# Performance work log

Hardware: AMD Instinct MI355X
Metric: run time of the kernel (lower is better)

## Reference

```python
import jax, jax.numpy as jnp
import numpy as np

N, DEG, C_IN, C_OUT = 100000, 16, 128, 128
LN_EPS = 1e-5


def setup_inputs() -> dict:
    key = jax.random.key(0)
    k1, k2, k3, k4 = jax.random.split(key, 4)
    x = jax.random.normal(k1, (N, C_IN), dtype=jnp.float32)
    # padding index == N points at the appended zero row
    edge_index = jax.random.randint(k2, (N, DEG), 0, N + 1)
    W = jax.random.normal(k3, (C_IN, C_OUT), dtype=jnp.float32) * 0.05
    b = jax.random.normal(k4, (C_OUT,), dtype=jnp.float32) * 0.05
    eps = jnp.zeros((1,), dtype=jnp.float32)
    gamma = jnp.ones((C_OUT,), dtype=jnp.float32)
    beta = jnp.zeros((C_OUT,), dtype=jnp.float32)
    return {"x": x, "edge_index": edge_index, "W": W, "b": b,
            "eps": eps, "gamma": gamma, "beta": beta}


def reference(x, edge_index, W, b, eps, gamma, beta):
    # pad with a zero row so padding index N gathers zeros
    padded = jnp.concatenate([x, jnp.zeros((1, x.shape[1]), x.dtype)], axis=0)  # [N+1, C]
    neigh = padded[edge_index]                 # [N, DEG, C] irregular gather
    agg = neigh.sum(axis=1)                    # [N, C] neighbor sum
    h = (1.0 + eps) * x + agg                  # GIN combine
    h = h @ W + b                              # Linear
    # LayerNorm over last dim (affine, biased variance, eps=1e-5)
    mu = h.mean(axis=-1, keepdims=True)
    var = h.var(axis=-1, keepdims=True)
    out = (h - mu) * jax.lax.rsqrt(var + LN_EPS) * gamma + beta
    return out
```

## Files before the change

### kernel.cpp

```cpp
#include <hip/hip_runtime.h>
#include <stdint.h>

#define NN   100000
#define DEG  16
#define CH   128
#define TILE 64

typedef __attribute__((ext_vector_type(8))) short bf16x8;
typedef __attribute__((ext_vector_type(4))) float f32x4;

__device__ __forceinline__ uint32_t pack2_bf16(float a, float b) {
    uint32_t ua = __builtin_bit_cast(uint32_t, a);
    uint32_t ub = __builtin_bit_cast(uint32_t, b);
    ua = (ua + 0x7FFFu + ((ua >> 16) & 1u)) >> 16;
    ub = (ub + 0x7FFFu + ((ub >> 16) & 1u)) >> 16;
    return ua | (ub << 16);
}
__device__ __forceinline__ float bf_lo(uint32_t w) { return __builtin_bit_cast(float, w << 16); }
__device__ __forceinline__ float bf_hi(uint32_t w) { return __builtin_bit_cast(float, w & 0xFFFF0000u); }

__global__ __launch_bounds__(256)
void convert_x_kernel(const float* __restrict__ x, uint32_t* __restrict__ xbf) {
    const int total = NN * CH / 8;
    for (int i = blockIdx.x * blockDim.x + threadIdx.x; i < total;
         i += gridDim.x * blockDim.x) {
        float4 a = ((const float4*)x)[2 * i];
        float4 b = ((const float4*)x)[2 * i + 1];
        uint4 o;
        o.x = pack2_bf16(a.x, a.y); o.y = pack2_bf16(a.z, a.w);
        o.z = pack2_bf16(b.x, b.y); o.w = pack2_bf16(b.z, b.w);
        ((uint4*)xbf)[i] = o;
    }
    if (blockIdx.x == 0 && threadIdx.x < CH / 8)
        ((uint4*)xbf)[NN * (CH / 8) + threadIdx.x] = make_uint4(0, 0, 0, 0);
}


template <int BF>
__global__ __launch_bounds__(256, 3)
void gin_fused_kernel(const float* __restrict__ x,
                      const uint32_t* __restrict__ xbf,
                      const int*   __restrict__ edge,
                      const float* __restrict__ W,
                      const float* __restrict__ bias,
                      const float* __restrict__ epsp,
                      const float* __restrict__ gamma,
                      const float* __restrict__ beta,
                      float*       __restrict__ out)
{
    __shared__ uint32_t Wl[128 * 64];
    __shared__ uint32_t Hl[TILE * 64];

    const int t    = threadIdx.x;
    const int lane = t & 63;
    const int wv   = t >> 6;
    const int cl   = lane & 15;
    const int g4   = lane >> 4;

    #pragma unroll
    for (int j = 0; j < 32; ++j) {
        int e  = t + 256 * j;
        int n  = e & 127;
        int k2 = e >> 7;
        float a = W[(2 * k2)     * CH + n];
        float c = W[(2 * k2 + 1) * CH + n];
        Wl[n * 64 + (k2 ^ ((n & 7) << 2))] = pack2_bf16(a, c);
    }

    const float eps1 = 1.0f + epsp[0];
    float g_r[8], be_r[8], bi_r[8];
    #pragma unroll
    for (int ct = 0; ct < 8; ++ct) {
        g_r[ct]  = gamma[ct * 16 + cl];
        be_r[ct] = beta [ct * 16 + cl];
        bi_r[ct] = bias [ct * 16 + cl];
    }

    const int tile_base = blockIdx.x * TILE;
    const uint4* xb4 = (const uint4*)xbf;

    #pragma unroll
    for (int it = 0; it < 4; ++it) {
        const int row  = 16 * wv + 4 * it + g4;
        const int node = tile_base + row;
        const bool nvalid = node < NN;
        int j_all = edge[(size_t)(nvalid ? node : 0) * DEG + cl];

        float acc[8] = {0, 0, 0, 0, 0, 0, 0, 0};
        #pragma unroll
        for (int d = 0; d < DEG; ++d) {
            int j = __shfl(j_all, g4 * 16 + d, 64);
            if (BF) {
                uint4 v = xb4[(size_t)j * (CH / 8) + cl];
                acc[0] += bf_lo(v.x); acc[1] += bf_hi(v.x);
                acc[2] += bf_lo(v.y); acc[3] += bf_hi(v.y);
                acc[4] += bf_lo(v.z); acc[5] += bf_hi(v.z);
                acc[6] += bf_lo(v.w); acc[7] += bf_hi(v.w);
            } else {
                bool ok = j < NN;
                size_t jc = ok ? (size_t)j : 0;
                float4 a = ((const float4*)x)[jc * (CH / 4) + cl * 2];
                float4 b = ((const float4*)x)[jc * (CH / 4) + cl * 2 + 1];
                float m = ok ? 1.0f : 0.0f;
                acc[0] += m * a.x; acc[1] += m * a.y;
                acc[2] += m * a.z; acc[3] += m * a.w;
                acc[4] += m * b.x; acc[5] += m * b.y;
                acc[6] += m * b.z; acc[7] += m * b.w;
            }
        }
        if (BF) {
            size_t nz = nvalid ? (size_t)node : (size_t)NN;
            uint4 v = xb4[nz * (CH / 8) + cl];
            acc[0] += eps1 * bf_lo(v.x); acc[1] += eps1 * bf_hi(v.x);
            acc[2] += eps1 * bf_lo(v.y); acc[3] += eps1 * bf_hi(v.y);
            acc[4] += eps1 * bf_lo(v.z); acc[5] += eps1 * bf_hi(v.z);
            acc[6] += eps1 * bf_lo(v.w); acc[7] += eps1 * bf_hi(v.w);
        } else if (nvalid) {
            float4 a = ((const float4*)x)[(size_t)node * (CH / 4) + cl * 2];
            float4 b = ((const float4*)x)[(size_t)node * (CH / 4) + cl * 2 + 1];
            acc[0] += eps1 * a.x; acc[1] += eps1 * a.y;
            acc[2] += eps1 * a.z; acc[3] += eps1 * a.w;
            acc[4] += eps1 * b.x; acc[5] += eps1 * b.y;
            acc[6] += eps1 * b.z; acc[7] += eps1 * b.w;
        }
        uint4 hv;
        hv.x = pack2_bf16(acc[0], acc[1]); hv.y = pack2_bf16(acc[2], acc[3]);
        hv.z = pack2_bf16(acc[4], acc[5]); hv.w = pack2_bf16(acc[6], acc[7]);
        int hidx = row * 64 + ((cl * 4) ^ ((row & 7) << 2));
        ((uint4*)Hl)[hidx >> 2] = hv;
    }
    __syncthreads();

    const int arow = 16 * wv + cl;
    bf16x8 afr[4];
    #pragma unroll
    for (int ks = 0; ks < 4; ++ks) {
        int k2b = ks * 16 + g4 * 4;
        afr[ks] = *reinterpret_cast<const bf16x8*>(&Hl[arow * 64 + (k2b ^ ((arow & 7) << 2))]);
    }
    f32x4 acc[8];
    #pragma unroll
    for (int ct = 0; ct < 8; ++ct) acc[ct] = (f32x4){0.f, 0.f, 0.f, 0.f};
    #pragma unroll
    for (int ct = 0; ct < 8; ++ct) {
        int brow = ct * 16 + cl;
        #pragma unroll
        for (int ks = 0; ks < 4; ++ks) {
            int k2b = ks * 16 + g4 * 4;
            bf16x8 bfr = *reinterpret_cast<const bf16x8*>(&Wl[brow * 64 + (k2b ^ ((brow & 7) << 2))]);
            acc[ct] = __builtin_amdgcn_mfma_f32_16x16x32_bf16(afr[ks], bfr, acc[ct], 0, 0, 0);
        }
    }

    float s1[4] = {0, 0, 0, 0}, s2[4] = {0, 0, 0, 0};
    #pragma unroll
    for (int ct = 0; ct < 8; ++ct) {
        #pragma unroll
        for (int r = 0; r < 4; ++r) {
            float v = acc[ct][r] + bi_r[ct];
            acc[ct][r] = v;
            s1[r] += v;
            s2[r] += v * v;
        }
    }
    #pragma unroll
    for (int m = 1; m < 16; m <<= 1) {
        #pragma unroll
        for (int r = 0; r < 4; ++r) {
            s1[r] += __shfl_xor(s1[r], m, 64);
            s2[r] += __shfl_xor(s2[r], m, 64);
        }
    }
    #pragma unroll
    for (int r = 0; r < 4; ++r) {
        int node = tile_base + 16 * wv + g4 * 4 + r;
        if (node < NN) {
            float mu  = s1[r] * (1.0f / CH);
            float var = s2[r] * (1.0f / CH) - mu * mu;
            float rs  = rsqrtf(var + 1e-5f);
            float* op = out + (size_t)node * CH + cl;
            #pragma unroll
            for (int ct = 0; ct < 8; ++ct) {
                op[ct * 16] = (acc[ct][r] - mu) * rs * g_r[ct] + be_r[ct];
            }
        }
    }
}

extern "C" void kernel_launch(void* const* d_in, const int* in_sizes, int n_in,
                              void* d_out, int out_size, void* d_ws, size_t ws_size,
                              hipStream_t stream) {
    const float* x     = (const float*)d_in[0];
    const int*   edge  = (const int*)  d_in[1];
    const float* W     = (const float*)d_in[2];
    const float* b     = (const float*)d_in[3];
    const float* eps   = (const float*)d_in[4];
    const float* gamma = (const float*)d_in[5];
    const float* beta  = (const float*)d_in[6];
    float*       out   = (float*)d_out;

    const int grid = (NN + TILE - 1) / TILE;
    const size_t need = (size_t)(NN + 1) * CH * 2;

    if (ws_size >= need) {
        uint32_t* xbf = (uint32_t*)d_ws;
        convert_x_kernel<<<2048, 256, 0, stream>>>(x, xbf);
        gin_fused_kernel<1><<<grid, 256, 0, stream>>>(x, xbf, edge, W, b, eps, gamma, beta, out);
    } else {
        gin_fused_kernel<0><<<grid, 256, 0, stream>>>(x, nullptr, edge, W, b, eps, gamma, beta, out);
    }
}
```

Measured before the change: 82.93 us.

## Pre-convert W to bf16 once and read MFMA B-fragments from global memory

The bf16 path no longer stages W into shared memory in every block. Block 1 of the convert kernel packs W into a bf16 buffer in the workspace, and the fused kernel loads its MFMA B fragments straight from that buffer, which should stay cache-resident. This removes 32KB of LDS and the per-block conversion, so launch_bounds is raised to 7 blocks per CU for higher occupancy, and all edge-index loads are hoisted ahead of the gather loop. The cost is global/L2 traffic for W fragments in every block, and whether the occupancy hint can be met under register pressure.

```diff
diff --git a/kernel.cpp b/kernel.cpp
--- a/kernel.cpp
+++ b/kernel.cpp
@@ -20,7 +20,8 @@
 __device__ __forceinline__ float bf_hi(uint32_t w) { return __builtin_bit_cast(float, w & 0xFFFF0000u); }
 
 __global__ __launch_bounds__(256)
-void convert_x_kernel(const float* __restrict__ x, uint32_t* __restrict__ xbf) {
+void convert_kernel(const float* __restrict__ x, const float* __restrict__ W,
+                    uint32_t* __restrict__ xbf, uint32_t* __restrict__ wbf) {
     const int total = NN * CH / 8;
     for (int i = blockIdx.x * blockDim.x + threadIdx.x; i < total;
          i += gridDim.x * blockDim.x) {
@@ -33,22 +34,29 @@
     }
     if (blockIdx.x == 0 && threadIdx.x < CH / 8)
         ((uint4*)xbf)[NN * (CH / 8) + threadIdx.x] = make_uint4(0, 0, 0, 0);
-}
-
-
-template <int BF>
-__global__ __launch_bounds__(256, 3)
-void gin_fused_kernel(const float* __restrict__ x,
-                      const uint32_t* __restrict__ xbf,
-                      const int*   __restrict__ edge,
-                      const float* __restrict__ W,
-                      const float* __restrict__ bias,
-                      const float* __restrict__ epsp,
-                      const float* __restrict__ gamma,
-                      const float* __restrict__ beta,
-                      float*       __restrict__ out)
+    if (blockIdx.x == 1) {
+        #pragma unroll
+        for (int j = 0; j < 32; ++j) {
+            int e  = threadIdx.x + 256 * j;
+            int n  = e & 127;
+            int k2 = e >> 7;
+            wbf[n * 64 + k2] = pack2_bf16(W[(2 * k2) * CH + n],
+                                          W[(2 * k2 + 1) * CH + n]);
+        }
+    }
+}
+
+
+__global__ __launch_bounds__(256, 7)
+void gin_fused_bf(const uint32_t* __restrict__ xbf,
+                  const uint32_t* __restrict__ wbf,
+                  const int*   __restrict__ edge,
+                  const float* __restrict__ bias,
+                  const float* __restrict__ epsp,
+                  const float* __restrict__ gamma,
+                  const float* __restrict__ beta,
+                  float*       __restrict__ out)
 {
-    __shared__ uint32_t Wl[128 * 64];
     __shared__ uint32_t Hl[TILE * 64];
 
     const int t    = threadIdx.x;
@@ -57,16 +65,6 @@
     const int cl   = lane & 15;
     const int g4   = lane >> 4;
 
-    #pragma unroll
-    for (int j = 0; j < 32; ++j) {
-        int e  = t + 256 * j;
-        int n  = e & 127;
-        int k2 = e >> 7;
-        float a = W[(2 * k2)     * CH + n];
-        float c = W[(2 * k2 + 1) * CH + n];
-        Wl[n * 64 + (k2 ^ ((n & 7) << 2))] = pack2_bf16(a, c);
-    }
-
     const float eps1 = 1.0f + epsp[0];
     float g_r[8], be_r[8], bi_r[8];
     #pragma unroll
@@ -79,50 +77,34 @@
     const int tile_base = blockIdx.x * TILE;
     const uint4* xb4 = (const uint4*)xbf;
 
+    int jv[4];
+    #pragma unroll
+    for (int it = 0; it < 4; ++it) {
+        int node = tile_base + 16 * wv + 4 * it + g4;
+        jv[it] = edge[(size_t)(node < NN ? node : 0) * DEG + cl];
+    }
+
     #pragma unroll
     for (int it = 0; it < 4; ++it) {
         const int row  = 16 * wv + 4 * it + g4;
         const int node = tile_base + row;
-        const bool nvalid = node < NN;
-        int j_all = edge[(size_t)(nvalid ? node : 0) * DEG + cl];
-
         float acc[8] = {0, 0, 0, 0, 0, 0, 0, 0};
         #pragma unroll
         for (int d = 0; d < DEG; ++d) {
-            int j = __shfl(j_all, g4 * 16 + d, 64);
-            if (BF) {
-                uint4 v = xb4[(size_t)j * (CH / 8) + cl];
-                acc[0] += bf_lo(v.x); acc[1] += bf_hi(v.x);
-                acc[2] += bf_lo(v.y); acc[3] += bf_hi(v.y);
-                acc[4] += bf_lo(v.z); acc[5] += bf_hi(v.z);
-                acc[6] += bf_lo(v.w); acc[7] += bf_hi(v.w);
-            } else {
-                bool ok = j < NN;
-                size_t jc = ok ? (size_t)j : 0;
-                float4 a = ((const float4*)x)[jc * (CH / 4) + cl * 2];
-                float4 b = ((const float4*)x)[jc * (CH / 4) + cl * 2 + 1];
-                float m = ok ? 1.0f : 0.0f;
-                acc[0] += m * a.x; acc[1] += m * a.y;
-                acc[2] += m * a.z; acc[3] += m * a.w;
-                acc[4] += m * b.x; acc[5] += m * b.y;
-                acc[6] += m * b.z; acc[7] += m * b.w;
-            }
-        }
-        if (BF) {
-            size_t nz = nvalid ? (size_t)node : (size_t)NN;
-            uint4 v = xb4[nz * (CH / 8) + cl];
-            acc[0] += eps1 * bf_lo(v.x); acc[1] += eps1 * bf_hi(v.x);
-            acc[2] += eps1 * bf_lo(v.y); acc[3] += eps1 * bf_hi(v.y);
-            acc[4] += eps1 * bf_lo(v.z); acc[5] += eps1 * bf_hi(v.z);
-            acc[6] += eps1 * bf_lo(v.w); acc[7] += eps1 * bf_hi(v.w);
-        } else if (nvalid) {
-            float4 a = ((const float4*)x)[(size_t)node * (CH / 4) + cl * 2];
-            float4 b = ((const float4*)x)[(size_t)node * (CH / 4) + cl * 2 + 1];
-            acc[0] += eps1 * a.x; acc[1] += eps1 * a.y;
-            acc[2] += eps1 * a.z; acc[3] += eps1 * a.w;
-            acc[4] += eps1 * b.x; acc[5] += eps1 * b.y;
-            acc[6] += eps1 * b.z; acc[7] += eps1 * b.w;
-        }
+            int j = __shfl(jv[it], g4 * 16 + d, 64);
+            uint4 v = xb4[(size_t)j * (CH / 8) + cl];
+            acc[0] += bf_lo(v.x); acc[1] += bf_hi(v.x);
+            acc[2] += bf_lo(v.y); acc[3] += bf_hi(v.y);
+            acc[4] += bf_lo(v.z); acc[5] += bf_hi(v.z);
+            acc[6] += bf_lo(v.w); acc[7] += bf_hi(v.w);
+        }
+        size_t nz = (node < NN) ? (size_t)node : (size_t)NN;
+        uint4 v = xb4[nz * (CH / 8) + cl];
+        acc[0] += eps1 * bf_lo(v.x); acc[1] += eps1 * bf_hi(v.x);
+        acc[2] += eps1 * bf_lo(v.y); acc[3] += eps1 * bf_hi(v.y);
+        acc[4] += eps1 * bf_lo(v.z); acc[5] += eps1 * bf_hi(v.z);
+        acc[6] += eps1 * bf_lo(v.w); acc[7] += eps1 * bf_hi(v.w);
+
         uint4 hv;
         hv.x = pack2_bf16(acc[0], acc[1]); hv.y = pack2_bf16(acc[2], acc[3]);
         hv.z = pack2_bf16(acc[4], acc[5]); hv.w = pack2_bf16(acc[6], acc[7]);
@@ -147,7 +129,7 @@
         #pragma unroll
         for (int ks = 0; ks < 4; ++ks) {
             int k2b = ks * 16 + g4 * 4;
-            bf16x8 bfr = *reinterpret_cast<const bf16x8*>(&Wl[brow * 64 + (k2b ^ ((brow & 7) << 2))]);
+            bf16x8 bfr = *reinterpret_cast<const bf16x8*>(&wbf[brow * 64 + k2b]);
             acc[ct] = __builtin_amdgcn_mfma_f32_16x16x32_bf16(afr[ks], bfr, acc[ct], 0, 0, 0);
         }
     }
@@ -187,6 +169,132 @@
     }
 }
 
+__global__ __launch_bounds__(256, 3)
+void gin_fused_f32(const float* __restrict__ x,
+                   const int*   __restrict__ edge,
+                   const float* __restrict__ W,
+                   const float* __restrict__ bias,
+                   const float* __restrict__ epsp,
+                   const float* __restrict__ gamma,
+                   const float* __restrict__ beta,
+                   float*       __restrict__ out)
+{
+    __shared__ uint32_t Wl[128 * 64];
+    __shared__ uint32_t Hl[TILE * 64];
+
+    const int t    = threadIdx.x;
+    const int lane = t & 63;
+    const int wv   = t >> 6;
+    const int cl   = lane & 15;
+    const int g4   = lane >> 4;
+
+    #pragma unroll
+    for (int j = 0; j < 32; ++j) {
+        int e  = t + 256 * j;
+        int n  = e & 127;
+        int k2 = e >> 7;
+        Wl[n * 64 + (k2 ^ ((n & 7) << 2))] =
+            pack2_bf16(W[(2 * k2) * CH + n], W[(2 * k2 + 1) * CH + n]);
+    }
+    const float eps1 = 1.0f + epsp[0];
+    float g_r[8], be_r[8], bi_r[8];
+    #pragma unroll
+    for (int ct = 0; ct < 8; ++ct) {
+        g_r[ct]  = gamma[ct * 16 + cl];
+        be_r[ct] = beta [ct * 16 + cl];
+        bi_r[ct] = bias [ct * 16 + cl];
+    }
+    const int tile_base = blockIdx.x * TILE;
+    #pragma unroll
+    for (int it = 0; it < 4; ++it) {
+        const int row  = 16 * wv + 4 * it + g4;
+        const int node = tile_base + row;
+        const bool nvalid = node < NN;
+        int j_all = edge[(size_t)(nvalid ? node : 0) * DEG + cl];
+        float acc[8] = {0, 0, 0, 0, 0, 0, 0, 0};
+        #pragma unroll
+        for (int d = 0; d < DEG; ++d) {
+            int j = __shfl(j_all, g4 * 16 + d, 64);
+            bool ok = j < NN;
+            size_t jc = ok ? (size_t)j : 0;
+            float4 a = ((const float4*)x)[jc * (CH / 4) + cl * 2];
+            float4 b = ((const float4*)x)[jc * (CH / 4) + cl * 2 + 1];
+            float m = ok ? 1.0f : 0.0f;
+            acc[0] += m * a.x; acc[1] += m * a.y;
+            acc[2] += m * a.z; acc[3] += m * a.w;
+            acc[4] += m * b.x; acc[5] += m * b.y;
+            acc[6] += m * b.z; acc[7] += m * b.w;
+        }
+        if (nvalid) {
+            float4 a = ((const float4*)x)[(size_t)node * (CH / 4) + cl * 2];
+            float4 b = ((const float4*)x)[(size_t)node * (CH / 4) + cl * 2 + 1];
+            acc[0] += eps1 * a.x; acc[1] += eps1 * a.y;
+            acc[2] += eps1 * a.z; acc[3] += eps1 * a.w;
+            acc[4] += eps1 * b.x; acc[5] += eps1 * b.y;
+            acc[6] += eps1 * b.z; acc[7] += eps1 * b.w;
+        }
+        uint4 hv;
+        hv.x = pack2_bf16(acc[0], acc[1]); hv.y = pack2_bf16(acc[2], acc[3]);
+        hv.z = pack2_bf16(acc[4], acc[5]); hv.w = pack2_bf16(acc[6], acc[7]);
+        int hidx = row * 64 + ((cl * 4) ^ ((row & 7) << 2));
+        ((uint4*)Hl)[hidx >> 2] = hv;
+    }
+    __syncthreads();
+    const int arow = 16 * wv + cl;
+    bf16x8 afr[4];
+    #pragma unroll
+    for (int ks = 0; ks < 4; ++ks) {
+        int k2b = ks * 16 + g4 * 4;
+        afr[ks] = *reinterpret_cast<const bf16x8*>(&Hl[arow * 64 + (k2b ^ ((arow & 7) << 2))]);
+    }
+    f32x4 acc[8];
+    #pragma unroll
+    for (int ct = 0; ct < 8; ++ct) acc[ct] = (f32x4){0.f, 0.f, 0.f, 0.f};
+    #pragma unroll
+    for (int ct = 0; ct < 8; ++ct) {
+        int brow = ct * 16 + cl;
+        #pragma unroll
+        for (int ks = 0; ks < 4; ++ks) {
+            int k2b = ks * 16 + g4 * 4;
+            bf16x8 bfr = *reinterpret_cast<const bf16x8*>(&Wl[brow * 64 + (k2b ^ ((brow & 7) << 2))]);
+            acc[ct] = __builtin_amdgcn_mfma_f32_16x16x32_bf16(afr[ks], bfr, acc[ct], 0, 0, 0);
+        }
+    }
+    float s1[4] = {0, 0, 0, 0}, s2[4] = {0, 0, 0, 0};
+    #pragma unroll
+    for (int ct = 0; ct < 8; ++ct) {
+        #pragma unroll
+        for (int r = 0; r < 4; ++r) {
+            float v = acc[ct][r] + bi_r[ct];
+            acc[ct][r] = v;
+            s1[r] += v;
+            s2[r] += v * v;
+        }
+    }
+    #pragma unroll
+    for (int m = 1; m < 16; m <<= 1) {
+        #pragma unroll
+        for (int r = 0; r < 4; ++r) {
+            s1[r] += __shfl_xor(s1[r], m, 64);
+            s2[r] += __shfl_xor(s2[r], m, 64);
+        }
+    }
+    #pragma unroll
+    for (int r = 0; r < 4; ++r) {
+        int node = tile_base + 16 * wv + g4 * 4 + r;
+        if (node < NN) {
+            float mu  = s1[r] * (1.0f / CH);
+            float var = s2[r] * (1.0f / CH) - mu * mu;
+            float rs  = rsqrtf(var + 1e-5f);
+            float* op = out + (size_t)node * CH + cl;
+            #pragma unroll
+            for (int ct = 0; ct < 8; ++ct) {
+                op[ct * 16] = (acc[ct][r] - mu) * rs * g_r[ct] + be_r[ct];
+            }
+        }
+    }
+}
+
 extern "C" void kernel_launch(void* const* d_in, const int* in_sizes, int n_in,
                               void* d_out, int out_size, void* d_ws, size_t ws_size,
                               hipStream_t stream) {
@@ -200,13 +308,15 @@
     float*       out   = (float*)d_out;
 
     const int grid = (NN + TILE - 1) / TILE;
-    const size_t need = (size_t)(NN + 1) * CH * 2;
+    const size_t xbf_bytes = (size_t)(NN + 1) * CH * 2;
+    const size_t need = xbf_bytes + (size_t)CH * CH * 2;
 
     if (ws_size >= need) {
         uint32_t* xbf = (uint32_t*)d_ws;
-        convert_x_kernel<<<2048, 256, 0, stream>>>(x, xbf);
-        gin_fused_kernel<1><<<grid, 256, 0, stream>>>(x, xbf, edge, W, b, eps, gamma, beta, out);
+        uint32_t* wbf = (uint32_t*)((char*)d_ws + xbf_bytes);
+        convert_kernel<<<2048, 256, 0, stream>>>(x, W, xbf, wbf);
+        gin_fused_bf<<<grid, 256, 0, stream>>>(xbf, wbf, edge, b, eps, gamma, beta, out);
     } else {
-        gin_fused_kernel<0><<<grid, 256, 0, stream>>>(x, nullptr, edge, W, b, eps, gamma, beta, out);
-    }
-}
+        gin_fused_f32<<<grid, 256, 0, stream>>>(x, edge, W, b, eps, gamma, beta, out);
+    }
+}
```

Result: slower. 110.6 us (+33.3%).
